# Kernel tuning notes

Hardware: AMD Instinct MI355X
Metric: run time of the kernel (lower is better)

The kernel has to match this reference:

```python
import jax, jax.numpy as jnp
import numpy as np
from jax import lax

B, N, FEAT, MID, HID, OUT = 128, 36, 2048, 517, 128, 1024
STEPS, TEMP = 3, 1.0


def setup_inputs() -> dict:
    key = jax.random.key(0)
    ks = jax.random.split(key, 10)
    s = 0.02
    return {
        "boxes": jax.random.uniform(ks[0], (B, 4, N), jnp.float32),
        "attention": jax.random.normal(ks[1], (B, N), jnp.float32),
        "features": jax.random.normal(ks[2], (B, N, FEAT), jnp.float32),
        "conv_w": jax.random.normal(ks[3], (MID - 5, FEAT), jnp.float32) * s,
        "conv_b": jnp.zeros((MID - 5,), jnp.float32),
        "skew_wx": jax.random.normal(ks[4], (HID, MID), jnp.float32) * s,
        "skew_wy": jax.random.normal(ks[5], (HID, MID), jnp.float32) * s,
        "skew_b1": jnp.zeros((HID,), jnp.float32),
        "skew_w2": jax.random.normal(ks[6], (HID,), jnp.float32) * s,
        "skew_b2": jnp.zeros((1,), jnp.float32),
        "w_ih": jax.random.normal(ks[7], (4 * OUT, MID), jnp.float32) * s,
        "w_hh": jax.random.normal(ks[8], (4 * OUT, OUT), jnp.float32) * s,
        "b_ih": jnp.zeros((4 * OUT,), jnp.float32),
        "b_hh": jnp.zeros((4 * OUT,), jnp.float32),
        "lr": jnp.ones((1,), jnp.float32),
    }


def _calculate_assignment(C, lr_abs, temp, steps):
    # C: (b, n, n) skew-symmetric ordering costs.
    logits = jnp.zeros_like(C)
    for _ in range(steps):
        P = jax.nn.softmax(logits / temp, axis=-1)  # position i -> distribution over elements l
        cum = jnp.cumsum(P, axis=1)                 # sum over positions k <= i
        below = cum - P                             # sum_{k<i} P_kl
        above = cum[:, -1:, :] - cum                # sum_{k>i} P_kl
        # grad_{ij} = sum_l C_{jl} * (above - below)_{il}  (uses skew-symmetry of C)
        G = jnp.einsum('bil,bjl->bij', above - below, C)
        logits = logits - lr_abs * G
    return jax.nn.softmax(logits / temp, axis=-1)


def reference(boxes, attention, features, conv_w, conv_b, skew_wx, skew_wy,
              skew_b1, skew_w2, skew_b2, w_ih, w_hh, b_ih, b_hh, lr):
    b = boxes.shape[0]
    # normalize boxes by per-sample max
    boxes = boxes / jnp.max(boxes.reshape(b, -1), axis=1)[:, None, None]
    # pointwise Conv1: 2048 -> MID-5, features arrives as (b, n, 2048)
    f = jnp.einsum('bnf,mf->bmn', features, conv_w) + conv_b[None, :, None]
    att = attention[:, None, :]                      # (b, 1, n)
    feats = jnp.concatenate([boxes, att, f], axis=1)  # (b, MID, n)
    # PairwiseSkew: f(x_i, x_j) - f(x_j, x_i); the first 1x1-conv over concatenated
    # pairs splits into two linear maps so we never materialize (b, 2*MID, n, n).
    hx = jnp.einsum('hm,bmn->bhn', skew_wx, feats)
    hy = jnp.einsum('hm,bmn->bhn', skew_wy, feats)
    h = jax.nn.relu(hx[:, :, :, None] + hy[:, :, None, :] + skew_b1[None, :, None, None])
    out = jnp.einsum('h,bhij->bij', skew_w2, h) + skew_b2[0]  # (b, n, n)
    C = out - jnp.swapaxes(out, 1, 2)  # skew-symmetrize
    A = _calculate_assignment(C, jnp.abs(lr)[0], TEMP, STEPS)
    # gate features by sigmoid(attention) and apply soft permutation
    gated = feats * jax.nn.sigmoid(att)               # (b, MID, n)
    x = jnp.einsum('bcl,bil->bci', gated, A)          # (b, MID, n)
    x_seq = jnp.transpose(x, (2, 0, 1))               # (n, b, MID)
    # single-layer LSTM (PyTorch gate order i, f, g, o); return final cell state
    bias = b_ih + b_hh
    Hd = w_hh.shape[1]
    def step(carry, xt):
        h_, c_ = carry
        gates = xt @ w_ih.T + h_ @ w_hh.T + bias
        i, fg, g, o = jnp.split(gates, 4, axis=-1)
        c_ = jax.nn.sigmoid(fg) * c_ + jax.nn.sigmoid(i) * jnp.tanh(g)
        h_ = jax.nn.sigmoid(o) * jnp.tanh(c_)
        return (h_, c_), None
    init = (jnp.zeros((b, Hd), x.dtype), jnp.zeros((b, Hd), x.dtype))
    (_, c_fin), _ = lax.scan(step, init, x_seq)
    return c_fin
```

## Files before the change

### kernel.cpp

```cpp
#include <hip/hip_runtime.h>
#include <math.h>

#define NB 128
#define NN 36
#define S37 37
#define S40 40
#define NFEAT 2048
#define NMID 517
#define KP 544
#define NHID 128
#define NOUT 1024
#define ROWS (NB*NN)

typedef __bf16 bf16x8 __attribute__((ext_vector_type(8)));
typedef float  f32x4  __attribute__((ext_vector_type(4)));

__device__ __forceinline__ float sigf(float x){ return 1.f/(1.f+expf(-x)); }
__device__ __forceinline__ unsigned short f2bf(float x){
    unsigned u = __float_as_uint(x);
    return (unsigned short)((u + 0x7FFFu + ((u>>16)&1u)) >> 16);
}
__device__ __forceinline__ float bf2f(unsigned short b){
    return __uint_as_float(((unsigned)b) << 16);
}
__device__ __forceinline__ void gload_lds16(const unsigned short* g, void* lds){
    __builtin_amdgcn_global_load_lds(
        (const __attribute__((address_space(1))) void*)g,
        (__attribute__((address_space(3))) void*)lds, 16, 0, 0);
}

__global__ __launch_bounds__(256) void prep_all(
    const float* __restrict__ boxes, const float* __restrict__ att,
    const float* __restrict__ features, const float* __restrict__ conv_w,
    const float* __restrict__ wx, const float* __restrict__ wy,
    const float* __restrict__ b1, const float* __restrict__ w_ih,
    const float* __restrict__ w_hh, const float* __restrict__ b_ih,
    const float* __restrict__ b_hh,
    unsigned short* __restrict__ features_bf, unsigned short* __restrict__ convw_bf,
    unsigned short* __restrict__ wxy_bf, float* __restrict__ hxy_b,
    unsigned short* __restrict__ wih_il, unsigned short* __restrict__ whh_il,
    float* __restrict__ comb_b, unsigned int* __restrict__ bar,
    float* __restrict__ feats)
{
    int gtid = blockIdx.x*256 + threadIdx.x;
    int gs = gridDim.x*256;
    if (gtid < 128*64) {
        int b = gtid >> 6, t = gtid & 63;
        float mx = -1e30f;
        for (int idx = t; idx < 4*NN; idx += 64) mx = fmaxf(mx, boxes[b*4*NN + idx]);
        for (int off = 32; off > 0; off >>= 1) mx = fmaxf(mx, __shfl_down(mx, off));
        mx = __shfl(mx, 0);
        float inv = 1.f / mx;
        for (int idx = t; idx < 4*NN; idx += 64) {
            int r = idx / NN, n = idx - r*NN;
            feats[(size_t)(b*NN+n)*NMID + r] = boxes[b*4*NN + idx] * inv;
        }
        if (t < NN) feats[(size_t)(b*NN+t)*NMID + 4] = att[b*NN + t];
    }
    for (int i = gtid; i < ROWS*NFEAT; i += gs) features_bf[i] = f2bf(features[i]);
    for (int i = gtid; i < 512*NFEAT; i += gs) convw_bf[i] = f2bf(conv_w[i]);
    for (int i = gtid; i < 256*KP; i += gs) {
        int r = i / KP, k = i - r*KP;
        float v = 0.f;
        if (k < NMID) v = (r < NHID) ? wx[(size_t)r*NMID+k] : wy[(size_t)(r-NHID)*NMID+k];
        wxy_bf[i] = f2bf(v);
    }
    for (int i = gtid; i < 256; i += gs) hxy_b[i] = (i < NHID) ? b1[i] : 0.f;
    for (int i = gtid; i < 4*NOUT*KP; i += gs) {
        int row = i / KP, k = i - row*KP;
        int u = row >> 2, g = row & 3;
        wih_il[i] = (k < NMID) ? f2bf(w_ih[(size_t)(g*NOUT+u)*NMID + k]) : (unsigned short)0;
    }
    for (int i = gtid; i < 4*NOUT*NOUT; i += gs) {
        int row = i >> 10, k = i & 1023;
        int u = row >> 2, g = row & 3;
        whh_il[i] = f2bf(w_hh[(size_t)(g*NOUT+u)*NOUT + k]);
    }
    for (int i = gtid; i < 4*NOUT; i += gs) {
        int u = i >> 2, g = i & 3;
        comb_b[i] = b_ih[g*NOUT+u] + b_hh[g*NOUT+u];
    }
    for (int i = gtid; i < 512; i += gs) bar[i] = 0u;
}

__global__ __launch_bounds__(256) void gemm128(
    const unsigned short* __restrict__ A, const unsigned short* __restrict__ B,
    const float* __restrict__ bias, void* __restrict__ Cp,
    int Ksl, int lda, int ldb, int ldc, int obf, long long pstride)
{
    __shared__ __align__(16) char As[16384];
    __shared__ __align__(16) char Bs[16384];
    int m0 = blockIdx.y * 128, n0 = blockIdx.x * 128;
    int kbeg = blockIdx.z * Ksl;
    int tid = threadIdx.x;
    int lane = tid & 63, wave = tid >> 6;
    int wm = wave >> 1, wn = wave & 1;
    int sw = ((lane>>4)<<8) + (((lane&15) ^ ((lane>>4)<<2))<<4);
    f32x4 acc[4][4];
    #pragma unroll
    for (int i = 0; i < 4; ++i)
        #pragma unroll
        for (int j = 0; j < 4; ++j) acc[i][j] = (f32x4){0.f,0.f,0.f,0.f};

    int gq = lane >> 4, sl = lane & 15;
    int rloc = sl ^ (gq << 2);
    int g0r = wave*2*16 + rloc, g1r = g0r + 16;
    const unsigned short* a0 = A + (size_t)(m0 + g0r)*lda + kbeg + gq*8;
    const unsigned short* a1 = A + (size_t)(m0 + g1r)*lda + kbeg + gq*8;
    const unsigned short* b0 = B + (size_t)(n0 + g0r)*ldb + kbeg + gq*8;
    const unsigned short* b1 = B + (size_t)(n0 + g1r)*ldb + kbeg + gq*8;
    char* asd0 = As + ((wave*2)<<10); char* asd1 = asd0 + 1024;
    char* bsd0 = Bs + ((wave*2)<<10); char* bsd1 = bsd0 + 1024;

    for (int k0 = 0; k0 < Ksl; k0 += 32) {
        gload_lds16(a0 + k0, asd0);
        gload_lds16(a1 + k0, asd1);
        gload_lds16(b0 + k0, bsd0);
        gload_lds16(b1 + k0, bsd1);
        __syncthreads();
        bf16x8 af[4], bfr[4];
        #pragma unroll
        for (int i = 0; i < 4; ++i) af[i]  = *(bf16x8*)(As + ((wm*4+i)<<10) + sw);
        #pragma unroll
        for (int j = 0; j < 4; ++j) bfr[j] = *(bf16x8*)(Bs + ((wn*4+j)<<10) + sw);
        #pragma unroll
        for (int i = 0; i < 4; ++i)
            #pragma unroll
            for (int j = 0; j < 4; ++j)
                acc[i][j] = __builtin_amdgcn_mfma_f32_16x16x32_bf16(af[i], bfr[j], acc[i][j], 0, 0, 0);
        __syncthreads();
    }
    int colf = lane & 15, rowq = lane >> 4;
    #pragma unroll
    for (int j = 0; j < 4; ++j) {
        int col = n0 + (wn*4+j)*16 + colf;
        float bv = bias ? bias[col] : 0.f;
        #pragma unroll
        for (int i = 0; i < 4; ++i) {
            #pragma unroll
            for (int reg = 0; reg < 4; ++reg) {
                int row = m0 + (wm*4+i)*16 + rowq*4 + reg;
                float v = acc[i][j][reg] + bv;
                if (obf) ((unsigned short*)Cp)[(size_t)row*ldc + col] = f2bf(v);
                else ((float*)Cp + (size_t)blockIdx.z*pstride)[(size_t)row*ldc + col] = v;
            }
        }
    }
}

__global__ __launch_bounds__(256) void conv_reduce(
    const float* __restrict__ part, const float* __restrict__ bias,
    float* __restrict__ feats, unsigned short* __restrict__ feats_bf)
{
    int gtid = blockIdx.x*256 + threadIdx.x;
    int gs = gridDim.x*256;
    const size_t PS = (size_t)ROWS * 512;
    for (int i = gtid; i < ROWS*512; i += gs) {
        int r = i >> 9, cc = i & 511;
        float s = part[i] + part[PS+i] + part[2*PS+i] + part[3*PS+i] + bias[cc];
        feats[(size_t)r*NMID + 5 + cc] = s;
        feats_bf[(size_t)r*KP + 5 + cc] = f2bf(s);
    }
    for (int i = gtid; i < ROWS*5; i += gs) {
        int r = i / 5, cc = i - r*5;
        feats_bf[(size_t)r*KP + cc] = f2bf(feats[(size_t)r*NMID + cc]);
    }
    for (int i = gtid; i < ROWS*27; i += gs) {
        int r = i / 27, cc = i - r*27;
        feats_bf[(size_t)r*KP + 517 + cc] = 0;
    }
}

__global__ __launch_bounds__(256) void gemm_mfma(
    const unsigned short* __restrict__ A, const unsigned short* __restrict__ B,
    const float* __restrict__ bias, void* __restrict__ Cp,
    int K, int lda, int ldb, int ldc, int obf)
{
    __shared__ __align__(16) char As[8192];
    __shared__ __align__(16) char Bs[4096];
    int m0 = blockIdx.y * 128, n0 = blockIdx.x * 64;
    int tid = threadIdx.x;
    int lane = tid & 63, wave = tid >> 6;
    int wm = wave >> 1, wn = wave & 1;
    f32x4 acc[4][2];
    #pragma unroll
    for (int i = 0; i < 4; ++i)
        #pragma unroll
        for (int j = 0; j < 2; ++j) acc[i][j] = (f32x4){0.f,0.f,0.f,0.f};

    int gq = lane >> 4, sl = lane & 15;
    int g0r = wave*2*16 + sl, g1r = g0r + 16;
    const unsigned short* a0 = A + (size_t)(m0 + g0r)*lda + gq*8;
    const unsigned short* a1 = A + (size_t)(m0 + g1r)*lda + gq*8;
    const unsigned short* bb0 = B + (size_t)(n0 + wave*16 + sl)*ldb + gq*8;
    char* asd0 = As + ((wave*2)<<10); char* asd1 = asd0 + 1024;
    char* bsd0 = Bs + (wave<<10);

    for (int k0 = 0; k0 < K; k0 += 32) {
        gload_lds16(a0 + k0, asd0);
        gload_lds16(a1 + k0, asd1);
        gload_lds16(bb0 + k0, bsd0);
        __syncthreads();
        bf16x8 af[4], bfr[2];
        #pragma unroll
        for (int i = 0; i < 4; ++i) af[i]  = *(bf16x8*)(As + ((wm*4+i)<<10) + (lane<<4));
        #pragma unroll
        for (int j = 0; j < 2; ++j) bfr[j] = *(bf16x8*)(Bs + ((wn*2+j)<<10) + (lane<<4));
        #pragma unroll
        for (int i = 0; i < 4; ++i)
            #pragma unroll
            for (int j = 0; j < 2; ++j)
                acc[i][j] = __builtin_amdgcn_mfma_f32_16x16x32_bf16(af[i], bfr[j], acc[i][j], 0, 0, 0);
        __syncthreads();
    }
    int colf = lane & 15, rowq = lane >> 4;
    #pragma unroll
    for (int j = 0; j < 2; ++j) {
        int col = n0 + (wn*2+j)*16 + colf;
        float bv = bias ? bias[col] : 0.f;
        #pragma unroll
        for (int i = 0; i < 4; ++i) {
            #pragma unroll
            for (int reg = 0; reg < 4; ++reg) {
                int row = m0 + (wm*4+i)*16 + rowq*4 + reg;
                float v = acc[i][j][reg] + bv;
                if (obf) ((unsigned short*)Cp)[(size_t)row*ldc + col] = f2bf(v);
                else     ((float*)Cp)[(size_t)row*ldc + col] = v;
            }
        }
    }
}

__global__ __launch_bounds__(256) void out_k(
    const float* __restrict__ hxy, const float* __restrict__ w2,
    float* __restrict__ out_g)
{
    __shared__ float s_hx[9*129], s_hy[NN*129], s_w2[NHID];
    int b = blockIdx.x, i0 = blockIdx.y * 9, tid = threadIdx.x;
    for (int i = tid; i < 9*NHID; i += 256) {
        int n = i >> 7, h = i & 127;
        s_hx[n*129+h] = hxy[(size_t)(b*NN+i0+n)*256 + h];
    }
    for (int i = tid; i < NN*NHID; i += 256) {
        int n = i >> 7, h = i & 127;
        s_hy[n*129+h] = hxy[(size_t)(b*NN+n)*256 + 128 + h];
    }
    if (tid < NHID) s_w2[tid] = w2[tid];
    __syncthreads();
    for (int idx = tid; idx < 9*NN; idx += 256) {
        int il = idx / NN, j = idx - il*NN;
        const float* px = &s_hx[il*129];
        const float* py = &s_hy[j*129];
        float s = 0.f;
        #pragma unroll 8
        for (int h = 0; h < NHID; ++h) s += s_w2[h] * fmaxf(px[h] + py[h], 0.f);
        out_g[(size_t)b*NN*NN + (i0+il)*NN + j] = s;
    }
}

__global__ __launch_bounds__(256) void iter_k(
    const float* __restrict__ out_g, const float* __restrict__ att,
    const float* __restrict__ lr, float* __restrict__ A_g)
{
    __shared__ __align__(16) float s_out[NN*S40], s_C[NN*S40], s_logits[NN*S40], s_P[NN*S40];
    __shared__ float s_sg[NN];
    int b = blockIdx.x, tid = threadIdx.x;
    for (int idx = tid; idx < NN*NN; idx += 256) {
        int i = idx / NN, j = idx - i*NN;
        s_out[i*S40+j] = out_g[(size_t)b*NN*NN + idx];
        s_logits[i*S40+j] = 0.f;
    }
    if (tid < NN) s_sg[tid] = sigf(att[b*NN + tid]);
    float lr_abs = fabsf(lr[0]);
    __syncthreads();
    for (int idx = tid; idx < NN*NN; idx += 256) {
        int i = idx / NN, j = idx - i*NN;
        s_C[i*S40+j] = s_out[i*S40+j] - s_out[j*S40+i];
    }
    __syncthreads();
    for (int it = 0; it < 3; ++it) {
        if (tid < NN) {
            int i = tid;
            float mx = -1e30f;
            for (int l = 0; l < NN; ++l) mx = fmaxf(mx, s_logits[i*S40+l]);
            float sum = 0.f;
            for (int l = 0; l < NN; ++l) { float e = expf(s_logits[i*S40+l]-mx); s_P[i*S40+l] = e; sum += e; }
            float inv = 1.f/sum;
            for (int l = 0; l < NN; ++l) s_P[i*S40+l] *= inv;
        }
        __syncthreads();
        if (tid < NN) {
            int l = tid;
            float S = 0.f;
            for (int i = 0; i < NN; ++i) S += s_P[i*S40+l];
            float cum = 0.f;
            for (int i = 0; i < NN; ++i) {
                float p = s_P[i*S40+l];
                cum += p;
                s_P[i*S40+l] = S - 2.f*cum + p;
            }
        }
        __syncthreads();
        for (int idx = tid; idx < NN*NN; idx += 256) {
            int i = idx / NN, j = idx - i*NN;
            const f32x4* Pp = (const f32x4*)&s_P[i*S40];
            const f32x4* Cc = (const f32x4*)&s_C[j*S40];
            float g = 0.f;
            #pragma unroll
            for (int q = 0; q < 9; ++q) {
                f32x4 a = Pp[q], bb = Cc[q];
                g += a[0]*bb[0] + a[1]*bb[1] + a[2]*bb[2] + a[3]*bb[3];
            }
            s_logits[i*S40+j] -= lr_abs * g;
        }
        __syncthreads();
    }
    if (tid < NN) {
        int i = tid;
        float mx = -1e30f;
        for (int l = 0; l < NN; ++l) mx = fmaxf(mx, s_logits[i*S40+l]);
        float sum = 0.f;
        for (int l = 0; l < NN; ++l) { float e = expf(s_logits[i*S40+l]-mx); s_P[i*S40+l] = e; sum += e; }
        float inv = 1.f/sum;
        for (int l = 0; l < NN; ++l)
            A_g[(size_t)b*NN*NN + i*NN + l] = s_P[i*S40+l] * inv * s_sg[l];
    }
}

__global__ __launch_bounds__(256) void xseq_k(
    const float* __restrict__ feats, const float* __restrict__ A_g,
    unsigned short* __restrict__ xseq)
{
    __shared__ float s_P[NN*S37];
    int b = blockIdx.x, half = blockIdx.y, tid = threadIdx.x;
    for (int idx = tid; idx < NN*NN; idx += 256) {
        int i = idx / NN, l = idx - i*NN;
        s_P[i*S37+l] = A_g[(size_t)b*NN*NN + idx];
    }
    __syncthreads();
    const float* fb = feats + (size_t)b*NN*NMID;
    int ncols = (half == 0 && tid < 32) ? 2 : 1;
    #pragma unroll
    for (int rep = 0; rep < 2; ++rep) {
        if (rep >= ncols) break;
        int c = (rep == 0) ? half*256 + tid : 512 + tid;
        float colv[NN];
        #pragma unroll
        for (int l = 0; l < NN; ++l) colv[l] = (c < NMID) ? fb[l*NMID + c] : 0.f;
        #pragma unroll 4
        for (int i = 0; i < NN; ++i) {
            float s = 0.f;
            #pragma unroll
            for (int l = 0; l < NN; ++l) s += s_P[i*S37+l] * colv[l];
            xseq[((size_t)i*NB + b)*KP + c] = f2bf(s);
        }
    }
}

__global__ __launch_bounds__(256, 2) void lstm_persist(
    const unsigned short* __restrict__ whh, const unsigned short* __restrict__ xw,
    unsigned short* __restrict__ hseq, float* __restrict__ dout,
    unsigned int* __restrict__ bar)
{
    __shared__ __align__(16) char Bls[65536];
    __shared__ __align__(16) float gates[32][36];
    int tid = threadIdx.x, lane = tid & 63, wave = tid >> 6;
    int bt = blockIdx.x >> 7, ct = blockIdx.x & 127;
    int m0 = bt * 32, n0 = ct * 32;
    #pragma unroll
    for (int r = 0; r < 16; ++r) {
        int idx = r*256 + tid;
        int n = idx >> 7, kc = idx & 127;
        uint4 v = *(const uint4*)(whh + (size_t)(n0+n)*NOUT + kc*8);
        *(uint4*)(Bls + kc*512 + (((n&16) | ((n^kc)&15))<<4)) = v;
    }
    int wm = wave >> 1, wn = wave & 1;
    int q = lane >> 4, ml = lane & 15;
    int nl = wn*16 + ml;
    int ul = tid & 7, bl = tid >> 3;
    int b = m0 + bl, u = ct*8 + ul;
    unsigned int* flags = bar + bt*128;
    int fidx = lane & 31;
    float cc = 0.f;
    __syncthreads();
    for (int t = 0; t < NN; ++t) {
        uint2 xw2 = *(const uint2*)(xw + ((size_t)t*NB + b)*4*NOUT + n0 + ul*4);
        float g0 = bf2f((unsigned short)(xw2.x & 0xffffu));
        float g1 = bf2f((unsigned short)(xw2.x >> 16));
        float g2 = bf2f((unsigned short)(xw2.y & 0xffffu));
        float g3 = bf2f((unsigned short)(xw2.y >> 16));
        if (t > 0) {
            const unsigned short* hrow = hseq + (size_t)(t-1)*NB*NOUT
                                       + (size_t)(m0 + wm*16 + ml)*NOUT + q*8;
            f32x4 acc = (f32x4){0.f,0.f,0.f,0.f};
            unsigned tgt = (unsigned)t;
            bf16x8 abuf[2][8];
            for (;;) {
                unsigned f = __hip_atomic_load(flags + fidx,
                                  __ATOMIC_RELAXED, __HIP_MEMORY_SCOPE_AGENT);
                if (__all(f >= tgt)) break;
                __builtin_amdgcn_s_sleep(1);
            }
            asm volatile("" ::: "memory");
            #pragma unroll
            for (int i = 0; i < 8; ++i)
                abuf[0][i] = *(const bf16x8*)(hrow + i*32);
            #pragma unroll
            for (int c = 0; c < 4; ++c) {
                if (c < 3) {
                    for (;;) {
                        unsigned f = __hip_atomic_load(flags + 32*(c+1) + fidx,
                                          __ATOMIC_RELAXED, __HIP_MEMORY_SCOPE_AGENT);
                        if (__all(f >= tgt)) break;
                        __builtin_amdgcn_s_sleep(1);
                    }
                    asm volatile("" ::: "memory");
                    #pragma unroll
                    for (int i = 0; i < 8; ++i)
                        abuf[(c+1)&1][i] = *(const bf16x8*)(hrow + ((c+1)*8 + i)*32);
                }
                #pragma unroll
                for (int it2 = 0; it2 < 8; ++it2) {
                    int kc = (c*8 + it2)*4 + q;
                    bf16x8 bb = *(const bf16x8*)(Bls + kc*512 + (((nl&16) | ((nl^kc)&15))<<4));
                    acc = __builtin_amdgcn_mfma_f32_16x16x32_bf16(abuf[c&1][it2], bb, acc, 0, 0, 0);
                }
            }
            #pragma unroll
            for (int reg = 0; reg < 4; ++reg)
                gates[wm*16 + q*4 + reg][wn*16 + ml] = acc[reg];
            __syncthreads();
            float4 gl = *(const float4*)&gates[bl][ul*4];
            g0 += gl.x; g1 += gl.y; g2 += gl.z; g3 += gl.w;
        }
        float ig = sigf(g0), fg = sigf(g1), gg = tanhf(g2), og = sigf(g3);
        cc = fg*cc + ig*gg;
        if (t == NN-1) {
            dout[(size_t)b*NOUT + u] = cc;
        } else {
            unsigned short hb = f2bf(og*tanhf(cc));
            unsigned partner = (unsigned)__shfl_down((int)(unsigned)hb, 1);
            if ((ul & 1) == 0) {
                unsigned word = (unsigned)hb | (partner << 16);
                unsigned* dst = (unsigned*)(hseq + (size_t)t*NB*NOUT
                                            + (size_t)b*NOUT + u);
                __hip_atomic_store(dst, word, __ATOMIC_RELAXED,
                                   __HIP_MEMORY_SCOPE_AGENT);
            }
            asm volatile("s_waitcnt vmcnt(0)" ::: "memory");
            __syncthreads();
            if (tid == 0)
                __hip_atomic_store(flags + ct, (unsigned)(t + 1),
                                   __ATOMIC_RELAXED, __HIP_MEMORY_SCOPE_AGENT);
        }
    }
}

extern "C" void kernel_launch(void* const* d_in, const int* in_sizes, int n_in,
                              void* d_out, int out_size, void* d_ws, size_t ws_size,
                              hipStream_t stream) {
    (void)in_sizes; (void)n_in; (void)out_size; (void)ws_size;
    const float* boxes     = (const float*)d_in[0];
    const float* attention = (const float*)d_in[1];
    const float* features  = (const float*)d_in[2];
    const float* conv_w    = (const float*)d_in[3];
    const float* conv_b    = (const float*)d_in[4];
    const float* skew_wx   = (const float*)d_in[5];
    const float* skew_wy   = (const float*)d_in[6];
    const float* skew_b1   = (const float*)d_in[7];
    const float* skew_w2   = (const float*)d_in[8];
    const float* w_ih      = (const float*)d_in[10];
    const float* w_hh      = (const float*)d_in[11];
    const float* b_ih      = (const float*)d_in[12];
    const float* b_hh      = (const float*)d_in[13];
    const float* lr        = (const float*)d_in[14];

    char* ws = (char*)d_ws;
    float*          part     = (float*)(ws);
    unsigned short* xw_bf    = (unsigned short*)(ws);
    unsigned short* features_bf = (unsigned short*)(ws + 37748736);
    unsigned short* hseq     = (unsigned short*)(ws + 37748736);
    unsigned short* convw_bf = (unsigned short*)(ws + 56623104);
    float*          feats    = (float*)(ws + 58720256);
    float*          hxy      = (float*)(ws + 68249600);
    unsigned short* feats_bf = (unsigned short*)(ws + 72968192);
    unsigned short* xseq_bf  = (unsigned short*)(ws + 77981696);
    unsigned short* wih_il   = (unsigned short*)(ws + 82995200);
    unsigned short* whh_il   = (unsigned short*)(ws + 87451648);
    unsigned short* wxy_bf   = (unsigned short*)(ws + 95840256);
    float*          comb_b   = (float*)(ws + 96118784);
    float*          hxy_b    = (float*)(ws + 96135168);
    float*          out_g    = (float*)(ws + 96660480);
    float*          A_g      = (float*)(ws + 97324032);
    unsigned int*   bar      = (unsigned int*)(ws + 97987584);

    prep_all<<<2048, 256, 0, stream>>>(boxes, attention, features, conv_w,
                                       skew_wx, skew_wy, skew_b1, w_ih, w_hh,
                                       b_ih, b_hh, features_bf, convw_bf,
                                       wxy_bf, hxy_b, wih_il, whh_il, comb_b,
                                       bar, feats);
    gemm128<<<dim3(4, 36, 4), 256, 0, stream>>>(features_bf, convw_bf, nullptr,
                                                (void*)part, 512, NFEAT, NFEAT, 512, 0,
                                                (long long)ROWS*512);
    conv_reduce<<<2048, 256, 0, stream>>>(part, conv_b, feats, feats_bf);
    gemm_mfma<<<dim3(4, 36), 256, 0, stream>>>(feats_bf, wxy_bf, hxy_b,
                                               (void*)hxy, KP, KP, KP, 256, 0);
    out_k<<<dim3(NB, 4), 256, 0, stream>>>(hxy, skew_w2, out_g);
    iter_k<<<NB, 256, 0, stream>>>(out_g, attention, lr, A_g);
    xseq_k<<<dim3(NB, 2), 256, 0, stream>>>(feats, A_g, xseq_bf);
    gemm128<<<dim3(32, 36, 1), 256, 0, stream>>>(xseq_bf, wih_il, comb_b,
                                                 (void*)xw_bf, KP, KP, KP, 4*NOUT, 1, 0);
    lstm_persist<<<512, 256, 0, stream>>>(whh_il, xw_bf, hseq,
                                          (float*)d_out, bar);
}
```

Before: 644.1 us.

## Vectorize bf16 weight conversion and fuse skew cost, assignment, and permutation kernels

```diff
diff --git a/kernel.cpp b/kernel.cpp
--- a/kernel.cpp
+++ b/kernel.cpp
@@ -3,7 +3,6 @@
 
 #define NB 128
 #define NN 36
-#define S37 37
 #define S40 40
 #define NFEAT 2048
 #define NMID 517
@@ -22,6 +21,9 @@
 }
 __device__ __forceinline__ float bf2f(unsigned short b){
     return __uint_as_float(((unsigned)b) << 16);
+}
+__device__ __forceinline__ unsigned pack2(float a, float b){
+    return (unsigned)f2bf(a) | ((unsigned)f2bf(b) << 16);
 }
 __device__ __forceinline__ void gload_lds16(const unsigned short* g, void* lds){
     __builtin_amdgcn_global_load_lds(
@@ -57,8 +59,20 @@
         }
         if (t < NN) feats[(size_t)(b*NN+t)*NMID + 4] = att[b*NN + t];
     }
-    for (int i = gtid; i < ROWS*NFEAT; i += gs) features_bf[i] = f2bf(features[i]);
-    for (int i = gtid; i < 512*NFEAT; i += gs) convw_bf[i] = f2bf(conv_w[i]);
+    for (int i = gtid; i < ROWS*NFEAT/8; i += gs) {
+        const float* s = features + (size_t)i*8;
+        float4 v0 = *(const float4*)s, v1 = *(const float4*)(s+4);
+        uint4 o = { pack2(v0.x,v0.y), pack2(v0.z,v0.w),
+                    pack2(v1.x,v1.y), pack2(v1.z,v1.w) };
+        *(uint4*)(features_bf + (size_t)i*8) = o;
+    }
+    for (int i = gtid; i < 512*NFEAT/8; i += gs) {
+        const float* s = conv_w + (size_t)i*8;
+        float4 v0 = *(const float4*)s, v1 = *(const float4*)(s+4);
+        uint4 o = { pack2(v0.x,v0.y), pack2(v0.z,v0.w),
+                    pack2(v1.x,v1.y), pack2(v1.z,v1.w) };
+        *(uint4*)(convw_bf + (size_t)i*8) = o;
+    }
     for (int i = gtid; i < 256*KP; i += gs) {
         int r = i / KP, k = i - r*KP;
         float v = 0.f;
@@ -66,15 +80,26 @@
         wxy_bf[i] = f2bf(v);
     }
     for (int i = gtid; i < 256; i += gs) hxy_b[i] = (i < NHID) ? b1[i] : 0.f;
-    for (int i = gtid; i < 4*NOUT*KP; i += gs) {
-        int row = i / KP, k = i - row*KP;
+    for (int i = gtid; i < 4*NOUT*(KP/8); i += gs) {
+        int row = i / (KP/8), kb = i - row*(KP/8);
         int u = row >> 2, g = row & 3;
-        wih_il[i] = (k < NMID) ? f2bf(w_ih[(size_t)(g*NOUT+u)*NMID + k]) : (unsigned short)0;
-    }
-    for (int i = gtid; i < 4*NOUT*NOUT; i += gs) {
-        int row = i >> 10, k = i & 1023;
+        int base = kb*8;
+        const float* s = w_ih + (size_t)(g*NOUT+u)*NMID + base;
+        float f[8];
+        #pragma unroll
+        for (int t = 0; t < 8; ++t) f[t] = (base+t < NMID) ? s[t] : 0.f;
+        uint4 o = { pack2(f[0],f[1]), pack2(f[2],f[3]),
+                    pack2(f[4],f[5]), pack2(f[6],f[7]) };
+        *(uint4*)(wih_il + (size_t)row*KP + base) = o;
+    }
+    for (int i = gtid; i < 4*NOUT*NOUT/8; i += gs) {
+        int row = i >> 7, kb = i & 127;
         int u = row >> 2, g = row & 3;
-        whh_il[i] = f2bf(w_hh[(size_t)(g*NOUT+u)*NOUT + k]);
+        const float* s = w_hh + ((size_t)(g*NOUT+u) << 10) + kb*8;
+        float4 v0 = *(const float4*)s, v1 = *(const float4*)(s+4);
+        uint4 o = { pack2(v0.x,v0.y), pack2(v0.z,v0.w),
+                    pack2(v1.x,v1.y), pack2(v1.z,v1.w) };
+        *(uint4*)(whh_il + ((size_t)row << 10) + kb*8) = o;
     }
     for (int i = gtid; i < 4*NOUT; i += gs) {
         int u = i >> 2, g = i & 3;
@@ -231,51 +256,41 @@
     }
 }
 
-__global__ __launch_bounds__(256) void out_k(
+__global__ __launch_bounds__(256) void assign_k(
     const float* __restrict__ hxy, const float* __restrict__ w2,
-    float* __restrict__ out_g)
+    const float* __restrict__ att, const float* __restrict__ lr,
+    const float* __restrict__ feats, unsigned short* __restrict__ xseq)
 {
-    __shared__ float s_hx[9*129], s_hy[NN*129], s_w2[NHID];
-    int b = blockIdx.x, i0 = blockIdx.y * 9, tid = threadIdx.x;
-    for (int i = tid; i < 9*NHID; i += 256) {
-        int n = i >> 7, h = i & 127;
-        s_hx[n*129+h] = hxy[(size_t)(b*NN+i0+n)*256 + h];
-    }
+    __shared__ float s_hx[NN*129], s_hy[NN*129], s_w2[NHID], s_sg[NN];
+    __shared__ __align__(16) float s_C[NN*S40], s_logits[NN*S40], s_P[NN*S40];
+    int b = blockIdx.x, tid = threadIdx.x;
     for (int i = tid; i < NN*NHID; i += 256) {
         int n = i >> 7, h = i & 127;
+        s_hx[n*129+h] = hxy[(size_t)(b*NN+n)*256 + h];
         s_hy[n*129+h] = hxy[(size_t)(b*NN+n)*256 + 128 + h];
     }
     if (tid < NHID) s_w2[tid] = w2[tid];
-    __syncthreads();
-    for (int idx = tid; idx < 9*NN; idx += 256) {
-        int il = idx / NN, j = idx - il*NN;
-        const float* px = &s_hx[il*129];
-        const float* py = &s_hy[j*129];
-        float s = 0.f;
-        #pragma unroll 8
-        for (int h = 0; h < NHID; ++h) s += s_w2[h] * fmaxf(px[h] + py[h], 0.f);
-        out_g[(size_t)b*NN*NN + (i0+il)*NN + j] = s;
-    }
-}
-
-__global__ __launch_bounds__(256) void iter_k(
-    const float* __restrict__ out_g, const float* __restrict__ att,
-    const float* __restrict__ lr, float* __restrict__ A_g)
-{
-    __shared__ __align__(16) float s_out[NN*S40], s_C[NN*S40], s_logits[NN*S40], s_P[NN*S40];
-    __shared__ float s_sg[NN];
-    int b = blockIdx.x, tid = threadIdx.x;
-    for (int idx = tid; idx < NN*NN; idx += 256) {
-        int i = idx / NN, j = idx - i*NN;
-        s_out[i*S40+j] = out_g[(size_t)b*NN*NN + idx];
-        s_logits[i*S40+j] = 0.f;
-    }
     if (tid < NN) s_sg[tid] = sigf(att[b*NN + tid]);
     float lr_abs = fabsf(lr[0]);
     __syncthreads();
     for (int idx = tid; idx < NN*NN; idx += 256) {
         int i = idx / NN, j = idx - i*NN;
-        s_C[i*S40+j] = s_out[i*S40+j] - s_out[j*S40+i];
+        const float* px = &s_hx[i*129];
+        const float* py = &s_hy[j*129];
+        float s = 0.f;
+        #pragma unroll 8
+        for (int h = 0; h < NHID; ++h) s += s_w2[h] * fmaxf(px[h] + py[h], 0.f);
+        s_logits[i*S40+j] = s;
+    }
+    __syncthreads();
+    for (int idx = tid; idx < NN*NN; idx += 256) {
+        int i = idx / NN, j = idx - i*NN;
+        s_C[i*S40+j] = s_logits[i*S40+j] - s_logits[j*S40+i];
+    }
+    __syncthreads();
+    for (int idx = tid; idx < NN*NN; idx += 256) {
+        int i = idx / NN, j = idx - i*NN;
+        s_logits[i*S40+j] = 0.f;
     }
     __syncthreads();
     for (int it = 0; it < 3; ++it) {
@@ -322,37 +337,24 @@
         float sum = 0.f;
         for (int l = 0; l < NN; ++l) { float e = expf(s_logits[i*S40+l]-mx); s_P[i*S40+l] = e; sum += e; }
         float inv = 1.f/sum;
-        for (int l = 0; l < NN; ++l)
-            A_g[(size_t)b*NN*NN + i*NN + l] = s_P[i*S40+l] * inv * s_sg[l];
-    }
-}
-
-__global__ __launch_bounds__(256) void xseq_k(
-    const float* __restrict__ feats, const float* __restrict__ A_g,
-    unsigned short* __restrict__ xseq)
-{
-    __shared__ float s_P[NN*S37];
-    int b = blockIdx.x, half = blockIdx.y, tid = threadIdx.x;
-    for (int idx = tid; idx < NN*NN; idx += 256) {
-        int i = idx / NN, l = idx - i*NN;
-        s_P[i*S37+l] = A_g[(size_t)b*NN*NN + idx];
+        for (int l = 0; l < NN; ++l) s_P[i*S40+l] *= inv * s_sg[l];
     }
     __syncthreads();
     const float* fb = feats + (size_t)b*NN*NMID;
-    int ncols = (half == 0 && tid < 32) ? 2 : 1;
     #pragma unroll
-    for (int rep = 0; rep < 2; ++rep) {
-        if (rep >= ncols) break;
-        int c = (rep == 0) ? half*256 + tid : 512 + tid;
-        float colv[NN];
-        #pragma unroll
-        for (int l = 0; l < NN; ++l) colv[l] = (c < NMID) ? fb[l*NMID + c] : 0.f;
-        #pragma unroll 4
-        for (int i = 0; i < NN; ++i) {
-            float s = 0.f;
-            #pragma unroll
-            for (int l = 0; l < NN; ++l) s += s_P[i*S37+l] * colv[l];
-            xseq[((size_t)i*NB + b)*KP + c] = f2bf(s);
+    for (int rep = 0; rep < 3; ++rep) {
+        int c = rep*256 + tid;
+        if (c < KP) {
+            float colv[NN];
+            #pragma unroll
+            for (int l = 0; l < NN; ++l) colv[l] = (c < NMID) ? fb[l*NMID + c] : 0.f;
+            #pragma unroll 4
+            for (int i = 0; i < NN; ++i) {
+                float s = 0.f;
+                #pragma unroll
+                for (int l = 0; l < NN; ++l) s += s_P[i*S40+l] * colv[l];
+                xseq[((size_t)i*NB + b)*KP + c] = f2bf(s);
+            }
         }
     }
 }
@@ -490,8 +492,6 @@
     unsigned short* wxy_bf   = (unsigned short*)(ws + 95840256);
     float*          comb_b   = (float*)(ws + 96118784);
     float*          hxy_b    = (float*)(ws + 96135168);
-    float*          out_g    = (float*)(ws + 96660480);
-    float*          A_g      = (float*)(ws + 97324032);
     unsigned int*   bar      = (unsigned int*)(ws + 97987584);
 
     prep_all<<<2048, 256, 0, stream>>>(boxes, attention, features, conv_w,
@@ -505,9 +505,8 @@
     conv_reduce<<<2048, 256, 0, stream>>>(part, conv_b, feats, feats_bf);
     gemm_mfma<<<dim3(4, 36), 256, 0, stream>>>(feats_bf, wxy_bf, hxy_b,
                                                (void*)hxy, KP, KP, KP, 256, 0);
-    out_k<<<dim3(NB, 4), 256, 0, stream>>>(hxy, skew_w2, out_g);
-    iter_k<<<NB, 256, 0, stream>>>(out_g, attention, lr, A_g);
-    xseq_k<<<dim3(NB, 2), 256, 0, stream>>>(feats, A_g, xseq_bf);
+    assign_k<<<NB, 256, 0, stream>>>(hxy, skew_w2, attention, lr,
+                                     feats, xseq_bf);
     gemm128<<<dim3(32, 36, 1), 256, 0, stream>>>(xseq_bf, wih_il, comb_b,
                                                  (void*)xw_bf, KP, KP, KP, 4*NOUT, 1, 0);
     lstm_persist<<<512, 256, 0, stream>>>(whh_il, xw_bf, hseq,
```

After: 640.7 us (median of 2 runs). About the same (-0.5%).
